# Kernel optimization log

Measured on AMD Instinct MI355X. Metric: run time of the kernel, lower is better.

The kernel has to match this reference:

```python
import jax, jax.numpy as jnp
import numpy as np

H = 512

def setup_inputs() -> dict:
    key = jax.random.key(0)
    k1, k2, k3 = jax.random.split(key, 3)
    encoder_outputs = jax.random.normal(k1, (32, 4096, H), dtype=jnp.float32)  # (B,T,H)
    W = jax.random.normal(k2, (H, H), dtype=jnp.float32) * (1.0 / np.sqrt(H))  # attn.weight
    v = jax.random.normal(k3, (H,), dtype=jnp.float32) * (1.0 / np.sqrt(H))    # v param
    return {"encoder_outputs": encoder_outputs, "W": W, "v": v}

def reference(encoder_outputs, W, v):
    # score: energy = tanh(x @ W.T); attn_energies = v . energy over H -> (B,T)
    energy = jnp.tanh(jnp.einsum('bth,gh->btg', encoder_outputs, W))
    attn_energies = jnp.einsum('btg,g->bt', energy, v)
    # method == 'bmm': softmax over T, weighted sum over T -> (B,H)
    attn_w = jax.nn.softmax(attn_energies, axis=-1)
    out = jnp.einsum('bt,bth->bh', attn_w, encoder_outputs)
    return out
```

## Files before the change

### kernel.cpp

```cpp
#include <hip/hip_runtime.h>
#include <hip/hip_bf16.h>

typedef __attribute__((ext_vector_type(8))) short short8;
typedef __attribute__((ext_vector_type(4))) float f32x4;

#define B_SZ 32
#define T_SZ 4096
#define H_SZ 512
#define NROWS (B_SZ * T_SZ)
#define RB 64

static __device__ __forceinline__ unsigned int pack2(float a, float b) {
  unsigned int r;
  asm("v_cvt_pk_bf16_f32 %0, %1, %2" : "=v"(r) : "v"(a), "v"(b));
  return r;
}
static __device__ __forceinline__ float fast_tanh(float x) {
  float e = __expf(2.0f * x);
  return 1.0f - 2.0f / (e + 1.0f);
}

__global__ __launch_bounds__(256) void prep_w_kernel(
    const float* __restrict__ W, uint4* __restrict__ Wfrag) {
  int s = blockIdx.x * 256 + threadIdx.x;
  int frow  = s & 15;
  int kslot = (s >> 4) & 3;
  int gf    = (s >> 6) & 31;
  int kc    = s >> 11;
  int g  = gf * 16 + frow;
  int k0 = kc * 32 + kslot * 8;
  const float4* Wf4 = reinterpret_cast<const float4*>(W);
  float4 lo = Wf4[g * 128 + (k0 >> 2)];
  float4 hi = Wf4[g * 128 + (k0 >> 2) + 1];
  uint4 u;
  u.x = pack2(lo.x, lo.y); u.y = pack2(lo.z, lo.w);
  u.z = pack2(hi.x, hi.y); u.w = pack2(hi.z, hi.w);
  Wfrag[s] = u;
}

__global__ __launch_bounds__(512, 4) void score_fused_kernel(
    const float* __restrict__ X, const uint4* __restrict__ Wfrag,
    const float* __restrict__ v,
    float* __restrict__ num, float2* __restrict__ md) {
  __shared__ unsigned char WsA[2][4096];
  __shared__ unsigned char WsB[2][32768];
  __shared__ float sp[4][RB];
  __shared__ float pLDS[RB];

  const int tid   = threadIdx.x;
  const int lane  = tid & 63;
  const int wave  = tid >> 6;
  const int frow  = lane & 15;
  const int kslot = lane >> 4;
  const int rg    = wave >> 2;
  const int gg    = wave & 3;
  const size_t rowbase = (size_t)blockIdx.x * RB;

  const int arow = tid >> 3;
  const int aqq  = tid & 7;
  const float4* Af4 = reinterpret_cast<const float4*>(X) + (rowbase + arow) * 128 + aqq;
  const int awoff = (arow >> 4) * 1024 + (((aqq >> 1) * 16 + (arow & 15)) << 4) + ((aqq & 1) << 3);

  #define STAGE_B(kc, buf)                                                      \
    {                                                                           \
      const char* src = (const char*)Wfrag + (size_t)(kc) * 32768 + tid * 16;   \
      unsigned char* dst = &WsB[buf][tid * 16];                                 \
      _Pragma("unroll")                                                         \
      for (int i = 0; i < 4; ++i)                                               \
        __builtin_amdgcn_global_load_lds((const unsigned int*)(src + i * 8192), \
                                         (unsigned int*)(dst + i * 8192), 16, 0, 0); \
    }
  #define WRITE_A(reg, buf)                                                     \
    {                                                                           \
      uint2 w2; w2.x = pack2((reg).x, (reg).y); w2.y = pack2((reg).z, (reg).w); \
      *reinterpret_cast<uint2*>(&WsA[buf][awoff]) = w2;                         \
    }

  float vv[8];
  #pragma unroll
  for (int j = 0; j < 8; ++j) vv[j] = v[(gg * 8 + j) * 16 + frow];

  float4 a0 = Af4[0];
  STAGE_B(0, 0);
  asm volatile("s_waitcnt vmcnt(0)" ::: "memory");
  WRITE_A(a0, 0);
  __syncthreads();

  f32x4 accA[8], accB[8];
  #pragma unroll
  for (int j = 0; j < 8; ++j) {
    accA[j] = (f32x4){0.f, 0.f, 0.f, 0.f};
    accB[j] = (f32x4){0.f, 0.f, 0.f, 0.f};
  }

  int cur = 0;
  for (int kc = 0; kc < 16; ++kc) {
    float4 a1;
    if (kc < 15) {
      a1 = Af4[(kc + 1) * 8];
      STAGE_B(kc + 1, cur ^ 1);
    }
    const unsigned char* pa = &WsA[cur][(rg * 2) * 1024 + lane * 16];
    short8 af0 = *reinterpret_cast<const short8*>(pa);
    short8 af1 = *reinterpret_cast<const short8*>(pa + 1024);
    const unsigned char* pb = &WsB[cur][(gg * 8) * 1024 + lane * 16];
    #pragma unroll
    for (int j = 0; j < 8; ++j) {
      short8 bf = *reinterpret_cast<const short8*>(pb + j * 1024);
      accA[j] = __builtin_amdgcn_mfma_f32_16x16x32_bf16(af0, bf, accA[j], 0, 0, 0);
      accB[j] = __builtin_amdgcn_mfma_f32_16x16x32_bf16(af1, bf, accB[j], 0, 0, 0);
    }
    if (kc < 15) {
      asm volatile("s_waitcnt vmcnt(0)" ::: "memory");
      WRITE_A(a1, cur ^ 1);
    }
    __syncthreads();
    cur ^= 1;
  }
  #undef STAGE_B
  #undef WRITE_A

  #pragma unroll
  for (int rs = 0; rs < 2; ++rs) {
    #pragma unroll
    for (int r = 0; r < 4; ++r) {
      float s = 0.f;
      #pragma unroll
      for (int j = 0; j < 8; ++j) {
        float e = (rs == 0) ? accA[j][r] : accB[j][r];
        s = fmaf(vv[j], fast_tanh(e), s);
      }
      #pragma unroll
      for (int d = 1; d < 16; d <<= 1) s += __shfl_xor(s, d);
      if (frow == 0) sp[gg][rg * 32 + rs * 16 + kslot * 4 + r] = s;
    }
  }
  __syncthreads();

  if (tid < 64) {
    float s = sp[0][tid] + sp[1][tid] + sp[2][tid] + sp[3][tid];
    float m = s;
    #pragma unroll
    for (int d = 1; d < 64; d <<= 1) m = fmaxf(m, __shfl_xor(m, d));
    float p = __expf(s - m);
    pLDS[tid] = p;
    float den = p;
    #pragma unroll
    for (int d = 1; d < 64; d <<= 1) den += __shfl_xor(den, d);
    if (tid == 0) {
      float2 r2; r2.x = m; r2.y = den;
      md[blockIdx.x] = r2;
    }
  }
  __syncthreads();

  {
    float a = 0.f;
    const float* xb = X + rowbase * H_SZ + tid;
    #pragma unroll 8
    for (int t = 0; t < RB; ++t)
      a = fmaf(pLDS[t], xb[(size_t)t * H_SZ], a);
    num[(size_t)blockIdx.x * H_SZ + tid] = a;
  }
}

__global__ __launch_bounds__(512) void combine_kernel(
    const float* __restrict__ num, const float2* __restrict__ md,
    float* __restrict__ out) {
  const int b = blockIdx.x;
  const int h = threadIdx.x;
  float M = -1e30f;
  #pragma unroll 8
  for (int c = 0; c < 64; ++c) M = fmaxf(M, md[b * 64 + c].x);
  float den = 0.f, acc = 0.f;
  #pragma unroll 4
  for (int c = 0; c < 64; ++c) {
    float2 m2 = md[b * 64 + c];
    float w = __expf(m2.x - M);
    den += w * m2.y;
    acc = fmaf(w, num[(size_t)(b * 64 + c) * H_SZ + h], acc);
  }
  out[b * H_SZ + h] = acc / den;
}

extern "C" void kernel_launch(void* const* d_in, const int* in_sizes, int n_in,
                              void* d_out, int out_size, void* d_ws, size_t ws_size,
                              hipStream_t stream) {
  const float* X = (const float*)d_in[0];
  const float* W = (const float*)d_in[1];
  const float* v = (const float*)d_in[2];
  float* out = (float*)d_out;
  unsigned char* ws = (unsigned char*)d_ws;

  uint4* Wfrag = (uint4*)(ws);
  float* num   = (float*)(ws + (512u << 10));
  float2* md   = (float2*)(ws + (512u << 10) + (4u << 20));

  prep_w_kernel<<<128, 256, 0, stream>>>(W, Wfrag);
  score_fused_kernel<<<NROWS / RB, 512, 0, stream>>>(X, Wfrag, v, num, md);
  combine_kernel<<<B_SZ, 512, 0, stream>>>(num, md, out);
}
```

Measured before the change: 155.1 us.

## Halve score block to four waves each computing all 64 rows

The fused score kernel now runs with 256 threads (4 waves), and each wave computes all four 16-row tiles of the 64-row block against its own 128-column slice. Each B fragment read from LDS therefore feeds four MFMAs instead of two, and the per-thread A and B staging loads double in width. The A write now waits only for its own loads (vmcnt(8)) before storing, and the final weighted sum uses float2 loads. This raises per-wave accumulator register use (32 f32x4) and halves the threads per block, which may change occupancy and latency hiding.

```diff
diff --git a/kernel.cpp b/kernel.cpp
--- a/kernel.cpp
+++ b/kernel.cpp
@@ -38,7 +38,7 @@
   Wfrag[s] = u;
 }
 
-__global__ __launch_bounds__(512, 4) void score_fused_kernel(
+__global__ __launch_bounds__(256, 2) void score_fused_kernel(
     const float* __restrict__ X, const uint4* __restrict__ Wfrag,
     const float* __restrict__ v,
     float* __restrict__ num, float2* __restrict__ md) {
@@ -49,90 +49,98 @@
 
   const int tid   = threadIdx.x;
   const int lane  = tid & 63;
-  const int wave  = tid >> 6;
+  const int gg    = tid >> 6;
   const int frow  = lane & 15;
   const int kslot = lane >> 4;
-  const int rg    = wave >> 2;
-  const int gg    = wave & 3;
   const size_t rowbase = (size_t)blockIdx.x * RB;
 
-  const int arow = tid >> 3;
-  const int aqq  = tid & 7;
-  const float4* Af4 = reinterpret_cast<const float4*>(X) + (rowbase + arow) * 128 + aqq;
-  const int awoff = (arow >> 4) * 1024 + (((aqq >> 1) * 16 + (arow & 15)) << 4) + ((aqq & 1) << 3);
+  const int arow = tid >> 2;
+  const int aqq  = tid & 3;
+  const float4* Af4 = reinterpret_cast<const float4*>(X) + (rowbase + arow) * 128 + aqq * 2;
+  const int awoff = (arow >> 4) * 1024 + ((aqq * 16 + (arow & 15)) << 4);
 
   #define STAGE_B(kc, buf)                                                      \
     {                                                                           \
       const char* src = (const char*)Wfrag + (size_t)(kc) * 32768 + tid * 16;   \
       unsigned char* dst = &WsB[buf][tid * 16];                                 \
       _Pragma("unroll")                                                         \
-      for (int i = 0; i < 4; ++i)                                               \
-        __builtin_amdgcn_global_load_lds((const unsigned int*)(src + i * 8192), \
-                                         (unsigned int*)(dst + i * 8192), 16, 0, 0); \
-    }
-  #define WRITE_A(reg, buf)                                                     \
+      for (int i = 0; i < 8; ++i)                                               \
+        __builtin_amdgcn_global_load_lds((const unsigned int*)(src + i * 4096), \
+                                         (unsigned int*)(dst + i * 4096), 16, 0, 0); \
+    }
+  #define WRITE_A(r0, r1, buf)                                                  \
     {                                                                           \
-      uint2 w2; w2.x = pack2((reg).x, (reg).y); w2.y = pack2((reg).z, (reg).w); \
-      *reinterpret_cast<uint2*>(&WsA[buf][awoff]) = w2;                         \
+      uint4 w4;                                                                 \
+      w4.x = pack2((r0).x, (r0).y); w4.y = pack2((r0).z, (r0).w);               \
+      w4.z = pack2((r1).x, (r1).y); w4.w = pack2((r1).z, (r1).w);               \
+      *reinterpret_cast<uint4*>(&WsA[buf][awoff]) = w4;                         \
     }
 
   float vv[8];
   #pragma unroll
   for (int j = 0; j < 8; ++j) vv[j] = v[(gg * 8 + j) * 16 + frow];
 
-  float4 a0 = Af4[0];
-  STAGE_B(0, 0);
-  asm volatile("s_waitcnt vmcnt(0)" ::: "memory");
-  WRITE_A(a0, 0);
+  {
+    float4 x0 = Af4[0];
+    float4 x1 = Af4[1];
+    STAGE_B(0, 0);
+    asm volatile("s_waitcnt vmcnt(0)" ::: "memory");
+    WRITE_A(x0, x1, 0);
+  }
   __syncthreads();
 
-  f32x4 accA[8], accB[8];
+  f32x4 acc[4][8];
   #pragma unroll
-  for (int j = 0; j < 8; ++j) {
-    accA[j] = (f32x4){0.f, 0.f, 0.f, 0.f};
-    accB[j] = (f32x4){0.f, 0.f, 0.f, 0.f};
-  }
-
-  int cur = 0;
+  for (int m = 0; m < 4; ++m)
+    #pragma unroll
+    for (int j = 0; j < 8; ++j)
+      acc[m][j] = (f32x4){0.f, 0.f, 0.f, 0.f};
+
   for (int kc = 0; kc < 16; ++kc) {
-    float4 a1;
+    const int buf = kc & 1;
+    float4 x0, x1;
     if (kc < 15) {
-      a1 = Af4[(kc + 1) * 8];
-      STAGE_B(kc + 1, cur ^ 1);
-    }
-    const unsigned char* pa = &WsA[cur][(rg * 2) * 1024 + lane * 16];
+      x0 = Af4[(kc + 1) * 8];
+      x1 = Af4[(kc + 1) * 8 + 1];
+      STAGE_B(kc + 1, buf ^ 1);
+    }
+
+    const unsigned char* pa = &WsA[buf][lane * 16];
+    const unsigned char* pb = &WsB[buf][(gg * 8) * 1024 + lane * 16];
     short8 af0 = *reinterpret_cast<const short8*>(pa);
     short8 af1 = *reinterpret_cast<const short8*>(pa + 1024);
-    const unsigned char* pb = &WsB[cur][(gg * 8) * 1024 + lane * 16];
+    short8 af2 = *reinterpret_cast<const short8*>(pa + 2048);
+    short8 af3 = *reinterpret_cast<const short8*>(pa + 3072);
     #pragma unroll
     for (int j = 0; j < 8; ++j) {
       short8 bf = *reinterpret_cast<const short8*>(pb + j * 1024);
-      accA[j] = __builtin_amdgcn_mfma_f32_16x16x32_bf16(af0, bf, accA[j], 0, 0, 0);
-      accB[j] = __builtin_amdgcn_mfma_f32_16x16x32_bf16(af1, bf, accB[j], 0, 0, 0);
-    }
+      acc[0][j] = __builtin_amdgcn_mfma_f32_16x16x32_bf16(af0, bf, acc[0][j], 0, 0, 0);
+      acc[1][j] = __builtin_amdgcn_mfma_f32_16x16x32_bf16(af1, bf, acc[1][j], 0, 0, 0);
+      acc[2][j] = __builtin_amdgcn_mfma_f32_16x16x32_bf16(af2, bf, acc[2][j], 0, 0, 0);
+      acc[3][j] = __builtin_amdgcn_mfma_f32_16x16x32_bf16(af3, bf, acc[3][j], 0, 0, 0);
+    }
+
     if (kc < 15) {
+      asm volatile("s_waitcnt vmcnt(8)" ::: "memory");
+      WRITE_A(x0, x1, buf ^ 1);
       asm volatile("s_waitcnt vmcnt(0)" ::: "memory");
-      WRITE_A(a1, cur ^ 1);
     }
     __syncthreads();
-    cur ^= 1;
   }
   #undef STAGE_B
   #undef WRITE_A
 
   #pragma unroll
-  for (int rs = 0; rs < 2; ++rs) {
+  for (int m = 0; m < 4; ++m) {
     #pragma unroll
     for (int r = 0; r < 4; ++r) {
       float s = 0.f;
       #pragma unroll
-      for (int j = 0; j < 8; ++j) {
-        float e = (rs == 0) ? accA[j][r] : accB[j][r];
-        s = fmaf(vv[j], fast_tanh(e), s);
-      }
+      for (int j = 0; j < 8; ++j)
+        s = fmaf(vv[j], fast_tanh(acc[m][j][r]), s);
       #pragma unroll
       for (int d = 1; d < 16; d <<= 1) s += __shfl_xor(s, d);
-      if (frow == 0) sp[gg][rg * 32 + rs * 16 + kslot * 4 + r] = s;
+      if (frow == 0) sp[gg][m * 16 + kslot * 4 + r] = s;
     }
   }
   __syncthreads();
@@ -155,12 +163,17 @@
   __syncthreads();
 
   {
-    float a = 0.f;
-    const float* xb = X + rowbase * H_SZ + tid;
+    float ax = 0.f, ay = 0.f;
+    const float2* xb = reinterpret_cast<const float2*>(X + rowbase * H_SZ) + tid;
     #pragma unroll 8
-    for (int t = 0; t < RB; ++t)
-      a = fmaf(pLDS[t], xb[(size_t)t * H_SZ], a);
-    num[(size_t)blockIdx.x * H_SZ + tid] = a;
+    for (int t = 0; t < RB; ++t) {
+      float p = pLDS[t];
+      float2 xv = xb[(size_t)t * (H_SZ / 2)];
+      ax = fmaf(p, xv.x, ax);
+      ay = fmaf(p, xv.y, ay);
+    }
+    float2 r; r.x = ax; r.y = ay;
+    reinterpret_cast<float2*>(num + (size_t)blockIdx.x * H_SZ)[tid] = r;
   }
 }
 
@@ -197,6 +210,6 @@
   float2* md   = (float2*)(ws + (512u << 10) + (4u << 20));
 
   prep_w_kernel<<<128, 256, 0, stream>>>(W, Wfrag);
-  score_fused_kernel<<<NROWS / RB, 512, 0, stream>>>(X, Wfrag, v, num, md);
+  score_fused_kernel<<<NROWS / RB, 256, 0, stream>>>(X, Wfrag, v, num, md);
   combine_kernel<<<B_SZ, 512, 0, stream>>>(num, md, out);
 }
```

After: 167.2 us. 7.8% more time.
